# Kernel tuning notes

Measured on AMD Instinct MI355X. Metric: run time of the kernel, lower is better.

Reference implementation:

```python
import jax, jax.numpy as jnp
import numpy as np

D_MODEL = 1024
D_STATE = 16
EXPAND = 2
D_INNER = EXPAND * D_MODEL
DT_RANK = 64  # ceil(1024/16)
D_CONV = 4


def setup_inputs() -> dict:
    key = jax.random.key(0)
    ks = jax.random.split(key, 8)
    s = 0.02
    x = jax.random.normal(ks[0], (2, 2048, D_MODEL), dtype=jnp.float32)
    W_in = jax.random.normal(ks[1], (D_MODEL, 2 * D_INNER), dtype=jnp.float32) * s
    W_conv = jax.random.normal(ks[2], (D_CONV, D_INNER), dtype=jnp.float32) * s  # depthwise taps
    b_conv = jnp.zeros((D_INNER,), dtype=jnp.float32)
    W_xproj = jax.random.normal(ks[3], (D_INNER, DT_RANK + 2 * D_STATE), dtype=jnp.float32) * s
    W_dt = jax.random.normal(ks[4], (DT_RANK, D_INNER), dtype=jnp.float32) * s
    b_dt = jnp.zeros((D_INNER,), dtype=jnp.float32)
    A_log = jnp.broadcast_to(jnp.log(jnp.arange(1, D_STATE + 1, dtype=jnp.float32)), (D_INNER, D_STATE))
    D = jnp.ones((D_INNER,), dtype=jnp.float32)
    W_out = jax.random.normal(ks[5], (D_INNER, D_MODEL), dtype=jnp.float32) * s
    return {"x": x, "W_in": W_in, "W_conv": W_conv, "b_conv": b_conv,
            "W_xproj": W_xproj, "W_dt": W_dt, "b_dt": b_dt,
            "A_log": A_log, "D": D, "W_out": W_out}


def _silu(v):
    return v * jax.nn.sigmoid(v)


def reference(x, W_in, W_conv, b_conv, W_xproj, W_dt, b_dt, A_log, D, W_out):
    B_, L, _ = x.shape
    xz = x @ W_in                     # [B, L, 2*d_inner]
    x_in, z = jnp.split(xz, 2, axis=-1)
    # causal depthwise conv1d (torch padding=d_conv-1 then slice to seq_len)
    pad = D_CONV - 1
    x_pad = jnp.pad(x_in, ((0, 0), (pad, 0), (0, 0)))
    x_conv = b_conv
    x_conv = sum(x_pad[:, k:k + L, :] * W_conv[k] for k in range(D_CONV)) + b_conv
    x_in = _silu(x_conv)              # [B, L, d_inner]
    dbc = x_in @ W_xproj
    dt = jax.nn.softplus(dbc[..., :DT_RANK] @ W_dt + b_dt)   # [B, L, d_inner]
    Bm = dbc[..., DT_RANK:DT_RANK + D_STATE]                  # [B, L, d_state]
    Cm = dbc[..., DT_RANK + D_STATE:]                          # [B, L, d_state]
    A = -jnp.exp(A_log)                                        # [d_inner, d_state]

    def step(state, inp):
        x_t, dt_t, B_t, C_t = inp   # [B,d_inner], [B,d_inner], [B,d_state], [B,d_state]
        dA = jnp.exp(jnp.clip(dt_t[:, :, None] * A[None], -10.0, 10.0))
        dB = dt_t[:, :, None] * B_t[:, None, :]
        state = jnp.clip(state * dA + x_t[:, :, None] * dB, -10.0, 10.0)
        y_t = jnp.einsum('bdn,bn->bd', state, C_t) + D * x_t
        return state, y_t

    tm = lambda a: jnp.swapaxes(a, 0, 1)  # time-major
    state0 = jnp.zeros((B_, D_INNER, D_STATE), dtype=x.dtype)
    _, ys = jax.lax.scan(step, state0, (tm(x_in), tm(dt), tm(Bm), tm(Cm)))
    y = jnp.swapaxes(ys, 0, 1)            # [B, L, d_inner]
    y = y * _silu(z)
    return y @ W_out                       # [B, L, d_model]
```

## Files before the change

### kernel.cpp

```cpp
#include <hip/hip_runtime.h>
#include <math.h>

#define D_MODEL 1024
#define D_INNER 2048
#define D_STATE 16
#define DT_RANK 64
#define LSEQ 2048
#define NBATCH 2
#define M_TOT (NBATCH * LSEQ)
#define DBC_STRIDE 128
#define CH 64
#define NCH (LSEQ / CH)
#define KSPL 8
#define OKSPL 2

typedef unsigned short ushort_t;
typedef unsigned int uint_t;
typedef __attribute__((ext_vector_type(8))) short bf16x8;
typedef __attribute__((ext_vector_type(4))) float f32x4;

__device__ __forceinline__ ushort_t f2bf_rne(float f) {
    uint_t u = __float_as_uint(f);
    u += 0x7fffu + ((u >> 16) & 1u);
    return (ushort_t)(u >> 16);
}
__device__ __forceinline__ float bf2f(ushort_t h) {
    return __uint_as_float(((uint_t)h) << 16);
}

template <int MODE, int TERMS>
__global__ __launch_bounds__(256) void gemm_bf16s(
    const ushort_t* __restrict__ Ah, const ushort_t* __restrict__ Al,
    const ushort_t* __restrict__ BTh, const ushort_t* __restrict__ BTl,
    float* __restrict__ C, float* __restrict__ AUX, int M, int N, int K)
{
    __shared__ __align__(16) ushort_t smem[4 * 128 * 32];
    ushort_t* sAh = smem;
    ushort_t* sAl = smem + 4096;
    ushort_t* sBh = smem + 8192;
    ushort_t* sBl = smem + 12288;
    const int tid = threadIdx.x;
    const int lane = tid & 63;
    const int m0 = blockIdx.y * 128;
    int ks = 0, nblk = blockIdx.x;
    if (MODE == 3) { ks = blockIdx.x; nblk = 0; }
    if (MODE == 4) { ks = blockIdx.x >> 3; nblk = blockIdx.x & 7; }
    const int n0 = nblk * 128;
    const int wave = tid >> 6;
    const int mw = (wave & 1) * 64, nw = (wave >> 1) * 64;
    const int fm = lane & 15, fk = lane >> 4;
    const int swz = fk ^ ((fm >> 1) & 3);

    f32x4 acc[4][4] = {};

    const int r_st0 = tid >> 2, cp0 = tid & 3;
    const int r_st1 = (256 + tid) >> 2, cp1 = tid & 3;
    const int cl0 = cp0 ^ ((r_st0 >> 1) & 3);
    const int cl1 = cp1 ^ ((r_st1 >> 1) & 3);
    const int ldsb0 = (tid & ~63) * 16;
    const int ldsb1 = (256 + (tid & ~63)) * 16;

    const int kbeg = (MODE == 3) ? ks * (K / KSPL)
                   : (MODE == 4) ? ks * (K / OKSPL) : 0;
    const int kend = (MODE == 3) ? kbeg + K / KSPL
                   : (MODE == 4) ? kbeg + K / OKSPL : K;

    for (int k0 = kbeg; k0 < kend; k0 += 32) {
        __syncthreads();
        {
            size_t ga0 = (size_t)(m0 + r_st0) * K + k0 + cl0 * 8;
            size_t ga1 = (size_t)(m0 + r_st1) * K + k0 + cl1 * 8;
            size_t gb0 = (size_t)(n0 + r_st0) * K + k0 + cl0 * 8;
            size_t gb1 = (size_t)(n0 + r_st1) * K + k0 + cl1 * 8;
            __builtin_amdgcn_global_load_lds(
                (const __attribute__((address_space(1))) void*)(Ah + ga0),
                (__attribute__((address_space(3))) void*)((char*)sAh + ldsb0), 16, 0, 0);
            __builtin_amdgcn_global_load_lds(
                (const __attribute__((address_space(1))) void*)(Ah + ga1),
                (__attribute__((address_space(3))) void*)((char*)sAh + ldsb1), 16, 0, 0);
            if (TERMS >= 3) {
                __builtin_amdgcn_global_load_lds(
                    (const __attribute__((address_space(1))) void*)(Al + ga0),
                    (__attribute__((address_space(3))) void*)((char*)sAl + ldsb0), 16, 0, 0);
                __builtin_amdgcn_global_load_lds(
                    (const __attribute__((address_space(1))) void*)(Al + ga1),
                    (__attribute__((address_space(3))) void*)((char*)sAl + ldsb1), 16, 0, 0);
            }
            __builtin_amdgcn_global_load_lds(
                (const __attribute__((address_space(1))) void*)(BTh + gb0),
                (__attribute__((address_space(3))) void*)((char*)sBh + ldsb0), 16, 0, 0);
            __builtin_amdgcn_global_load_lds(
                (const __attribute__((address_space(1))) void*)(BTh + gb1),
                (__attribute__((address_space(3))) void*)((char*)sBh + ldsb1), 16, 0, 0);
            if (TERMS >= 2) {
                __builtin_amdgcn_global_load_lds(
                    (const __attribute__((address_space(1))) void*)(BTl + gb0),
                    (__attribute__((address_space(3))) void*)((char*)sBl + ldsb0), 16, 0, 0);
                __builtin_amdgcn_global_load_lds(
                    (const __attribute__((address_space(1))) void*)(BTl + gb1),
                    (__attribute__((address_space(3))) void*)((char*)sBl + ldsb1), 16, 0, 0);
            }
        }
        __syncthreads();

        bf16x8 fAh[4], fAl[4], fBh[4], fBl[4];
        #pragma unroll
        for (int t = 0; t < 4; ++t) {
            int ra = (mw + t * 16 + fm) * 32 + swz * 8;
            int rb = (nw + t * 16 + fm) * 32 + swz * 8;
            fAh[t] = *reinterpret_cast<const bf16x8*>(&sAh[ra]);
            if (TERMS >= 3) fAl[t] = *reinterpret_cast<const bf16x8*>(&sAl[ra]);
            fBh[t] = *reinterpret_cast<const bf16x8*>(&sBh[rb]);
            if (TERMS >= 2) fBl[t] = *reinterpret_cast<const bf16x8*>(&sBl[rb]);
        }
        #pragma unroll
        for (int i = 0; i < 4; ++i)
            #pragma unroll
            for (int j = 0; j < 4; ++j) {
                acc[i][j] = __builtin_amdgcn_mfma_f32_16x16x32_bf16(fAh[i], fBh[j], acc[i][j], 0, 0, 0);
                if (TERMS >= 3)
                    acc[i][j] = __builtin_amdgcn_mfma_f32_16x16x32_bf16(fAl[i], fBh[j], acc[i][j], 0, 0, 0);
                if (TERMS >= 2)
                    acc[i][j] = __builtin_amdgcn_mfma_f32_16x16x32_bf16(fAh[i], fBl[j], acc[i][j], 0, 0, 0);
            }
    }

    float* Cq = (MODE == 3 || MODE == 4) ? C + (size_t)ks * M * N : C;
    #pragma unroll
    for (int i = 0; i < 4; ++i) {
        int row0 = m0 + mw + i * 16 + fk * 4;
        #pragma unroll
        for (int j = 0; j < 4; ++j) {
            int col = n0 + nw + j * 16 + fm;
            if (MODE == 2) {
                if (col < D_INNER) {
                    #pragma unroll
                    for (int r = 0; r < 4; ++r)
                        C[(size_t)(row0 + r) * D_INNER + col] = acc[i][j][r];
                } else {
                    float4 v = make_float4(acc[i][j][0], acc[i][j][1],
                                           acc[i][j][2], acc[i][j][3]);
                    *reinterpret_cast<float4*>(
                        &AUX[(size_t)(col - D_INNER) * M + row0]) = v;
                }
            } else if (MODE == 5) {
                const float* bias = (const float*)AUX;
                float bc_ = bias[col];
                f32x4 v;
                #pragma unroll
                for (int r = 0; r < 4; ++r) {
                    float t = acc[i][j][r] + bc_;
                    v[r] = fmaxf(t, 0.f) + log1pf(__expf(-fabsf(t)));
                }
                *reinterpret_cast<f32x4*>(&C[(size_t)col * M + row0]) = v;
            } else {
                #pragma unroll
                for (int r = 0; r < 4; ++r)
                    Cq[(size_t)(row0 + r) * N + col] = acc[i][j][r];
            }
        }
    }
}

__global__ __launch_bounds__(256) void xproj_red_k(
    const float* __restrict__ dbcp, float* __restrict__ dbc,
    float* __restrict__ BCT, ushort_t* __restrict__ dbch)
{
    int g = blockIdx.x * 256 + threadIdx.x;
    int m = g >> 7, c = g & 127;
    float s = 0.f;
    #pragma unroll
    for (int ks = 0; ks < KSPL; ++ks)
        s += dbcp[(size_t)ks * M_TOT * DBC_STRIDE + g];
    dbc[g] = s;
    if (c < 64)
        dbch[(size_t)m * 64 + c] = f2bf_rne(s);
    else if (c < 96)
        BCT[(size_t)(c - 64) * M_TOT + m] = s;
}

__global__ __launch_bounds__(256) void outred_k(
    const float* __restrict__ p, float* __restrict__ out)
{
    int i4 = (blockIdx.x * 256 + threadIdx.x) * 4;
    f32x4 a = *reinterpret_cast<const f32x4*>(p + i4);
    f32x4 b = *reinterpret_cast<const f32x4*>(p + (size_t)M_TOT * D_MODEL + i4);
    *reinterpret_cast<f32x4*>(out + i4) = a + b;
}

__global__ __launch_bounds__(256) void cast_h_k(
    const float* __restrict__ X, ushort_t* __restrict__ Xh)
{
    int i4 = (blockIdx.x * 256 + threadIdx.x) * 4;
    float4 v = *reinterpret_cast<const float4*>(X + i4);
    ushort2 a = make_ushort2(f2bf_rne(v.x), f2bf_rne(v.y));
    ushort2 b = make_ushort2(f2bf_rne(v.z), f2bf_rne(v.w));
    *reinterpret_cast<ushort2*>(Xh + i4)     = a;
    *reinterpret_cast<ushort2*>(Xh + i4 + 2) = b;
}

__global__ __launch_bounds__(256) void transpose_cast_k(
    const float* __restrict__ W, ushort_t* __restrict__ Th, ushort_t* __restrict__ Tl,
    int K, int N)
{
    __shared__ float tile[32][33];
    int n0 = blockIdx.x * 32, k0 = blockIdx.y * 32;
    int tx = threadIdx.x & 31, ty = threadIdx.x >> 5;
    #pragma unroll
    for (int i = 0; i < 32; i += 8)
        tile[ty + i][tx] = W[(size_t)(k0 + ty + i) * N + n0 + tx];
    __syncthreads();
    #pragma unroll
    for (int i = 0; i < 32; i += 8) {
        float v = tile[tx][ty + i];
        ushort_t h = f2bf_rne(v);
        ushort_t l = f2bf_rne(v - bf2f(h));
        size_t o = (size_t)(n0 + ty + i) * K + k0 + tx;
        Th[o] = h; Tl[o] = l;
    }
}

__global__ __launch_bounds__(256) void transpose_cast_pad_k(
    const float* __restrict__ W, ushort_t* __restrict__ Th, int K, int N)
{
    __shared__ float tile[32][33];
    int n0 = blockIdx.x * 32, k0 = blockIdx.y * 32;
    int tx = threadIdx.x & 31, ty = threadIdx.x >> 5;
    #pragma unroll
    for (int i = 0; i < 32; i += 8)
        tile[ty + i][tx] = (n0 + tx < N) ? W[(size_t)(k0 + ty + i) * N + n0 + tx] : 0.f;
    __syncthreads();
    #pragma unroll
    for (int i = 0; i < 32; i += 8) {
        float v = tile[tx][ty + i];
        size_t o = (size_t)(n0 + ty + i) * K + k0 + tx;
        Th[o] = f2bf_rne(v);
    }
}

__global__ __launch_bounds__(256) void conv_silu_k(
    const float* __restrict__ xbuf, const float* __restrict__ Wc,
    const float* __restrict__ bc, ushort_t* __restrict__ xinh,
    float* __restrict__ xT)
{
    __shared__ float tile[67][64];
    const int c0 = blockIdx.x * 64;
    const int m0 = blockIdx.y * 64;
    const int bstart = m0 & ~(LSEQ - 1);
    const int tid = threadIdx.x;

    for (int e = tid; e < 67 * 64; e += 256) {
        int r = e >> 6, c = e & 63;
        int g = m0 - 3 + r;
        tile[r][c] = (g >= bstart) ? xbuf[(size_t)g * D_INNER + c0 + c] : 0.f;
    }
    __syncthreads();

    const int c_l = tid & 63, mg = tid >> 6;
    const int c = c0 + c_l;
    const float w0 = Wc[c], w1 = Wc[D_INNER + c];
    const float w2 = Wc[2 * D_INNER + c], w3 = Wc[3 * D_INNER + c];
    const float bb = bc[c];
    float xtbuf[16];
    #pragma unroll
    for (int mi = 0; mi < 16; ++mi) {
        int r = mg * 16 + mi;
        float acc = bb + tile[r][c_l] * w0 + tile[r + 1][c_l] * w1
                       + tile[r + 2][c_l] * w2 + tile[r + 3][c_l] * w3;
        float sv = acc / (1.f + __expf(-acc));
        xinh[(size_t)(m0 + r) * D_INNER + c] = f2bf_rne(sv);
        xtbuf[mi] = sv;
    }
    float* xtp = xT + (size_t)c * M_TOT + m0 + mg * 16;
    #pragma unroll
    for (int q = 0; q < 4; ++q)
        *reinterpret_cast<float4*>(xtp + 4 * q) =
            make_float4(xtbuf[4 * q], xtbuf[4 * q + 1], xtbuf[4 * q + 2], xtbuf[4 * q + 3]);
}

__global__ __launch_bounds__(256) void scan_sum_k(
    const float* __restrict__ dtT, const float* __restrict__ xT,
    const float* __restrict__ BCT, const float* __restrict__ A_log,
    float* __restrict__ asumb, float* __restrict__ sendb)
{
    __shared__ float sdt[16][68], sx[16][68], sBs[16][68];
    const int tid = threadIdx.x;
    const int c0 = blockIdx.x << 4;
    const int ck = blockIdx.y;
    const int b  = blockIdx.z;
    const size_t boff = (size_t)b * LSEQ + ck * CH;

    {
        int r = tid >> 4, q = (tid & 15) << 2;
        *reinterpret_cast<float4*>(&sdt[r][q]) =
            *reinterpret_cast<const float4*>(dtT + (size_t)(c0 + r) * M_TOT + boff + q);
        *reinterpret_cast<float4*>(&sx[r][q]) =
            *reinterpret_cast<const float4*>(xT + (size_t)(c0 + r) * M_TOT + boff + q);
        *reinterpret_cast<float4*>(&sBs[r][q]) =
            *reinterpret_cast<const float4*>(BCT + (size_t)r * M_TOT + boff + q);
    }
    __syncthreads();

    const int n = tid & 15, ch = tid >> 4;
    const int d = c0 + ch;
    const float Adn = -__expf(A_log[d * D_STATE + n]);
    float s = 0.f, asum = 0.f;
    #pragma unroll 4
    for (int tq = 0; tq < CH / 4; ++tq) {
        f32x4 dv = *reinterpret_cast<const f32x4*>(&sdt[ch][tq * 4]);
        f32x4 xv = *reinterpret_cast<const f32x4*>(&sx[ch][tq * 4]);
        f32x4 Bv = *reinterpret_cast<const f32x4*>(&sBs[n][tq * 4]);
        #pragma unroll
        for (int j = 0; j < 4; ++j) {
            float a = fminf(fmaxf(dv[j] * Adn, -10.f), 10.f);
            asum += a;
            float e = __expf(a);
            float t = s * e + dv[j] * xv[j] * Bv[j];
            s = fminf(fmaxf(t, -10.f), 10.f);
        }
    }
    size_t idx = (((size_t)(b * NCH + ck) * D_INNER) + d) * D_STATE + n;
    asumb[idx] = asum;
    sendb[idx] = s;
}

__global__ __launch_bounds__(256) void scan_fix_k(
    const float* __restrict__ asumb, const float* __restrict__ sendb,
    float* __restrict__ sinb)
{
    int g = blockIdx.x * 256 + threadIdx.x;
    int n = g & 15, d = (g >> 4) & (D_INNER - 1), b = g >> 15;
    float s = 0.f;
    for (int ck = 0; ck < NCH; ++ck) {
        size_t idx = (((size_t)(b * NCH + ck) * D_INNER) + d) * D_STATE + n;
        sinb[idx] = s;
        float t = s * __expf(asumb[idx]) + sendb[idx];
        s = fminf(fmaxf(t, -10.f), 10.f);
    }
}

__global__ __launch_bounds__(256) void scan_apply_k(
    const float* __restrict__ dtT, const float* __restrict__ xT,
    const float* __restrict__ BCT, const float* __restrict__ zT,
    const float* __restrict__ sinb,
    const float* __restrict__ A_log, const float* __restrict__ Dv,
    ushort_t* __restrict__ Yh)
{
    __shared__ float sdt[16][68], sx[16][68], sBs[16][68], sCs[16][68], sz[16][68];
    __shared__ float ps[4][16 * 68];
    const int tid = threadIdx.x;
    const int c0 = blockIdx.x << 4;
    const int ck = blockIdx.y;
    const int b  = blockIdx.z;
    const size_t boff = (size_t)b * LSEQ + ck * CH;

    {
        int r = tid >> 4, q = (tid & 15) << 2;
        *reinterpret_cast<float4*>(&sdt[r][q]) =
            *reinterpret_cast<const float4*>(dtT + (size_t)(c0 + r) * M_TOT + boff + q);
        *reinterpret_cast<float4*>(&sx[r][q]) =
            *reinterpret_cast<const float4*>(xT + (size_t)(c0 + r) * M_TOT + boff + q);
        *reinterpret_cast<float4*>(&sBs[r][q]) =
            *reinterpret_cast<const float4*>(BCT + (size_t)r * M_TOT + boff + q);
        *reinterpret_cast<float4*>(&sCs[r][q]) =
            *reinterpret_cast<const float4*>(BCT + (size_t)(16 + r) * M_TOT + boff + q);
        *reinterpret_cast<float4*>(&sz[r][q]) =
            *reinterpret_cast<const float4*>(zT + (size_t)(c0 + r) * M_TOT + boff + q);
    }
    __syncthreads();

    const int w = tid >> 6, lane = tid & 63;
    const int n = lane & 15, cl = lane >> 4;
    const int t_r = lane >> 2, cl_r = lane & 3;
    const int chs = w * 4 + cl;
    const int d = c0 + chs;
    const int cho = w * 4 + cl_r;
    const int d_out = c0 + cho;
    const float Adn = -__expf(A_log[d * D_STATE + n]);
    const float DdEff = (n == 0) ? Dv[d] : 0.f;
    float s = sinb[(((size_t)(b * NCH + ck) * D_INNER) + d) * D_STATE + n];

    #pragma unroll
    for (int tg = 0; tg < CH / 16; ++tg) {
        #pragma unroll
        for (int tq = 0; tq < 4; ++tq) {
            int t4 = tg * 16 + tq * 4;
            f32x4 dv = *reinterpret_cast<const f32x4*>(&sdt[chs][t4]);
            f32x4 xv = *reinterpret_cast<const f32x4*>(&sx[chs][t4]);
            f32x4 Bv = *reinterpret_cast<const f32x4*>(&sBs[n][t4]);
            f32x4 Cv = *reinterpret_cast<const f32x4*>(&sCs[n][t4]);
            #pragma unroll
            for (int j = 0; j < 4; ++j) {
                float a = fminf(fmaxf(dv[j] * Adn, -10.f), 10.f);
                float e = __expf(a);
                float t = s * e + dv[j] * xv[j] * Bv[j];
                s = fminf(fmaxf(t, -10.f), 10.f);
                ps[w][(tq * 4 + j) * 68 + cl * 16 + n] = s * Cv[j] + DdEff * xv[j];
            }
        }
        __builtin_amdgcn_wave_barrier();
        {
            const float* pb = &ps[w][t_r * 68 + cl_r * 16];
            f32x4 r0 = *reinterpret_cast<const f32x4*>(pb + 0);
            f32x4 r1 = *reinterpret_cast<const f32x4*>(pb + 4);
            f32x4 r2 = *reinterpret_cast<const f32x4*>(pb + 8);
            f32x4 r3 = *reinterpret_cast<const f32x4*>(pb + 12);
            f32x4 sv4 = (r0 + r1) + (r2 + r3);
            float sum = (sv4[0] + sv4[1]) + (sv4[2] + sv4[3]);
            float zz = sz[cho][tg * 16 + t_r];
            float szg = zz / (1.f + __expf(-zz));
            float val = sum * szg;
            size_t om = (boff + tg * 16 + t_r) * D_INNER + d_out;
            Yh[om] = f2bf_rne(val);
        }
        __builtin_amdgcn_wave_barrier();
    }
}

extern "C" void kernel_launch(void* const* d_in, const int* in_sizes, int n_in,
                              void* d_out, int out_size, void* d_ws, size_t ws_size,
                              hipStream_t stream)
{
    const float* x       = (const float*)d_in[0];
    const float* W_in    = (const float*)d_in[1];
    const float* W_conv  = (const float*)d_in[2];
    const float* b_conv  = (const float*)d_in[3];
    const float* W_xproj = (const float*)d_in[4];
    const float* W_dt    = (const float*)d_in[5];
    const float* b_dt    = (const float*)d_in[6];
    const float* A_log   = (const float*)d_in[7];
    const float* Dv      = (const float*)d_in[8];
    const float* W_out   = (const float*)d_in[9];
    float* out = (float*)d_out;

    float* xbuf = (float*)d_ws;
    float* zT   = xbuf + (size_t)M_TOT * D_INNER;
    float* dbc  = zT + (size_t)D_INNER * M_TOT;
    float* BCT  = dbc + (size_t)M_TOT * DBC_STRIDE;
    ushort_t* xh     = (ushort_t*)(BCT + (size_t)32 * M_TOT);
    ushort_t* xl     = xh + (size_t)M_TOT * D_MODEL;
    ushort_t* WinTh  = xl + (size_t)M_TOT * D_MODEL;
    ushort_t* WinTl  = WinTh + (size_t)2 * D_INNER * D_MODEL;
    ushort_t* WoutTh = WinTl + (size_t)2 * D_INNER * D_MODEL;
    ushort_t* WoutTl = WoutTh + (size_t)D_MODEL * D_INNER;
    ushort_t* WxTh   = WoutTl + (size_t)D_MODEL * D_INNER;
    ushort_t* WxTl   = WxTh + (size_t)DBC_STRIDE * D_INNER;
    ushort_t* xinh   = WxTl + (size_t)DBC_STRIDE * D_INNER;
    ushort_t* xinl   = xinh + (size_t)M_TOT * D_INNER;
    ushort_t* yh     = xinl + (size_t)M_TOT * D_INNER;
    ushort_t* yl     = yh + (size_t)M_TOT * D_INNER;
    ushort_t* WdtTh  = yl + (size_t)M_TOT * D_INNER;
    ushort_t* dbch   = WdtTh + (size_t)D_INNER * DT_RANK;
    float* xT   = (float*)xh;
    float* dtT  = (float*)xinh;
    float* dbcp = (float*)yh;
    float* pout = (float*)xh;
    const size_t NSUM = (size_t)NBATCH * NCH * D_INNER * D_STATE;
    float* asumb = xbuf;
    float* sendb = xbuf + NSUM;
    float* sinb  = xbuf + 2 * NSUM;

    cast_h_k<<<(M_TOT * D_MODEL) / 1024, 256, 0, stream>>>(x, xh);
    transpose_cast_pad_k<<<dim3((2 * D_INNER) / 32, D_MODEL / 32), 256, 0, stream>>>(
        W_in, WinTh, D_MODEL, 2 * D_INNER);
    transpose_cast_k<<<dim3(D_MODEL / 32, D_INNER / 32), 256, 0, stream>>>(
        W_out, WoutTh, WoutTl, D_INNER, D_MODEL);
    transpose_cast_pad_k<<<dim3(DBC_STRIDE / 32, D_INNER / 32), 256, 0, stream>>>(
        W_xproj, WxTh, D_INNER, DT_RANK + 2 * D_STATE);
    transpose_cast_pad_k<<<dim3(D_INNER / 32, DT_RANK / 32), 256, 0, stream>>>(
        W_dt, WdtTh, DT_RANK, D_INNER);

    gemm_bf16s<2, 1><<<dim3(32, 32), 256, 0, stream>>>(
        xh, nullptr, WinTh, nullptr, xbuf, zT, M_TOT, 2 * D_INNER, D_MODEL);
    conv_silu_k<<<dim3(D_INNER / 64, M_TOT / 64), 256, 0, stream>>>(
        xbuf, W_conv, b_conv, xinh, xT);
    gemm_bf16s<3, 1><<<dim3(KSPL, 32), 256, 0, stream>>>(
        xinh, nullptr, WxTh, nullptr, dbcp, nullptr, M_TOT, DBC_STRIDE, D_INNER);
    xproj_red_k<<<(M_TOT * DBC_STRIDE) / 256, 256, 0, stream>>>(dbcp, dbc, BCT, dbch);
    gemm_bf16s<5, 1><<<dim3(D_INNER / 128, M_TOT / 128), 256, 0, stream>>>(
        dbch, nullptr, WdtTh, nullptr, dtT, (float*)b_dt, M_TOT, D_INNER, DT_RANK);
    scan_sum_k<<<dim3(D_INNER / 16, NCH, NBATCH), 256, 0, stream>>>(
        dtT, xT, BCT, A_log, asumb, sendb);
    scan_fix_k<<<(NBATCH * D_INNER * D_STATE) / 256, 256, 0, stream>>>(
        asumb, sendb, sinb);
    scan_apply_k<<<dim3(D_INNER / 16, NCH, NBATCH), 256, 0, stream>>>(
        dtT, xT, BCT, zT, sinb, A_log, Dv, yh);
    gemm_bf16s<4, 2><<<dim3(OKSPL * 8, 32), 256, 0, stream>>>(
        yh, nullptr, WoutTh, WoutTl, pout, nullptr, M_TOT, D_MODEL, D_INNER);
    outred_k<<<(M_TOT * D_MODEL) / 1024, 256, 0, stream>>>(pout, out);
}
```

Before: 380.9 us.

## Replace in-projection GEMM with 256x256-tile pipelined kernel using direct global-to-LDS loads

The input projection GEMM (4096x4096x1024, bf16 single term) moves from the generic 128x128 kernel to a dedicated 512-thread kernel with 256x256 tiles. It streams operands into LDS with global_load_lds in a double-buffered, multi-stage pipeline, using swizzled LDS layout, explicit vmcnt/lgkmcnt waits and setprio around MFMA bursts. The aim is more operand reuse per tile, with global loads overlapping the matrix math. In exchange it uses 128KB of LDS and only 256 blocks, and the hand-tuned wait counts are fragile.

```diff
diff --git a/kernel.cpp b/kernel.cpp
--- a/kernel.cpp
+++ b/kernel.cpp
@@ -26,6 +26,177 @@
 }
 __device__ __forceinline__ float bf2f(ushort_t h) {
     return __uint_as_float(((uint_t)h) << 16);
+}
+
+#define KIN 1024
+#define KTI (KIN / 64)
+
+#define BAR()   __builtin_amdgcn_s_barrier()
+#define LGKM0() asm volatile("s_waitcnt lgkmcnt(0)" ::: "memory")
+
+#define LDFRAG_B(SRC)                                                          \
+    _Pragma("unroll")                                                          \
+    for (int nf = 0; nf < 4; ++nf)                                             \
+        fB[nf] = *reinterpret_cast<const bf16x8*>(                             \
+            &(SRC)[(bRow + nf * 16 + fm) * 32 + swz * 8]);
+
+#define LDFRAG_A(SRC, MOFF)                                                    \
+    _Pragma("unroll")                                                          \
+    for (int mf = 0; mf < 4; ++mf)                                             \
+        fA[mf] = *reinterpret_cast<const bf16x8*>(                             \
+            &(SRC)[(aRow + (MOFF + mf) * 16 + fm) * 32 + swz * 8]);
+
+#define MFMA_QUAD(MOFF)                                                        \
+    __builtin_amdgcn_s_setprio(1);                                             \
+    _Pragma("unroll")                                                          \
+    for (int mf = 0; mf < 4; ++mf)                                             \
+        _Pragma("unroll")                                                      \
+        for (int nf = 0; nf < 4; ++nf)                                         \
+            acc[MOFF + mf][nf] = __builtin_amdgcn_mfma_f32_16x16x32_bf16(      \
+                fA[mf], fB[nf], acc[MOFF + mf][nf], 0, 0, 0);                  \
+    __builtin_amdgcn_s_setprio(0);
+
+__global__ __launch_bounds__(512, 2) void gemm256_inproj(
+    const ushort_t* __restrict__ Ah, const ushort_t* __restrict__ BTh,
+    float* __restrict__ C, float* __restrict__ AUX)
+{
+    __shared__ __align__(1024) ushort_t smem[65536];
+    const int tid  = threadIdx.x;
+    const int lane = tid & 63;
+    const int w    = tid >> 6;
+    const int wm   = w >> 2;
+    const int wn   = w & 3;
+    const int fm   = lane & 15, fk = lane >> 4;
+    const int swz  = fk ^ ((fm >> 1) & 3);
+    const int aRow = wm * 128;
+    const int bRow = wn * 64;
+    const int m0   = blockIdx.y * 256;
+    const int n0   = blockIdx.x * 256;
+    const int rbase = w * 16 + (lane >> 2);
+    const int ssw   = ((lane & 3) ^ ((lane >> 3) & 3)) * 8;
+
+    f32x4 acc[8][4] = {};
+
+    auto stage = [&](const ushort_t* __restrict__ g, int grow0, int kcol,
+                     int regUS) {
+        #pragma unroll
+        for (int q = 0; q < 2; ++q) {
+            const ushort_t* src =
+                g + (size_t)(grow0 + q * 128 + rbase) * KIN + kcol + ssw;
+            __builtin_amdgcn_global_load_lds(
+                (const __attribute__((address_space(1))) void*)src,
+                (__attribute__((address_space(3))) void*)(smem + regUS +
+                                                          q * 4096 + w * 512),
+                16, 0, 0);
+        }
+    };
+
+    stage(Ah,  m0, 0,  0);
+    stage(BTh, n0, 0,  32768);
+    stage(Ah,  m0, 32, 8192);
+    stage(BTh, n0, 32, 32768 + 8192);
+    stage(Ah,  m0, 64, 16384);
+    stage(BTh, n0, 64, 32768 + 16384);
+    asm volatile("s_waitcnt vmcnt(8)" ::: "memory");
+    BAR();
+
+    bf16x8 fA[4], fB[4];
+
+    for (int t = 0; t < KTI - 1; ++t) {
+        const int bf = t & 1, bn = bf ^ 1;
+        const ushort_t* A0 = smem + (bf * 2 + 0) * 8192;
+        const ushort_t* A1 = smem + (bf * 2 + 1) * 8192;
+        const ushort_t* B0 = smem + 32768 + (bf * 2 + 0) * 8192;
+        const ushort_t* B1 = smem + 32768 + (bf * 2 + 1) * 8192;
+        const int kc1 = (t + 1) * 64, kc2 = (t + 2) * 64;
+        const bool st2 = (t + 2 < KTI);
+
+        LDFRAG_B(B0);
+        LDFRAG_A(A0, 0);
+        stage(Ah, m0, kc1 + 32, (bn * 2 + 1) * 8192);
+        BAR(); LGKM0();
+        MFMA_QUAD(0);
+        BAR();
+
+        LDFRAG_A(A0, 4);
+        stage(BTh, n0, kc1 + 32, 32768 + (bn * 2 + 1) * 8192);
+        BAR(); LGKM0();
+        MFMA_QUAD(4);
+        asm volatile("s_waitcnt vmcnt(8)" ::: "memory");
+        BAR();
+        __builtin_amdgcn_sched_barrier(0);
+
+        LDFRAG_B(B1);
+        LDFRAG_A(A1, 0);
+        if (st2) stage(Ah, m0, kc2, (bf * 2 + 0) * 8192);
+        BAR(); LGKM0();
+        MFMA_QUAD(0);
+        BAR();
+
+        LDFRAG_A(A1, 4);
+        if (st2) stage(BTh, n0, kc2, 32768 + (bf * 2 + 0) * 8192);
+        BAR(); LGKM0();
+        MFMA_QUAD(4);
+        if (t == KTI - 2) { asm volatile("s_waitcnt vmcnt(4)" ::: "memory"); }
+        else              { asm volatile("s_waitcnt vmcnt(6)" ::: "memory"); }
+        BAR();
+        __builtin_amdgcn_sched_barrier(0);
+    }
+
+    {
+        const int bf = (KTI - 1) & 1;
+        const ushort_t* A0 = smem + (bf * 2 + 0) * 8192;
+        const ushort_t* A1 = smem + (bf * 2 + 1) * 8192;
+        const ushort_t* B0 = smem + 32768 + (bf * 2 + 0) * 8192;
+        const ushort_t* B1 = smem + 32768 + (bf * 2 + 1) * 8192;
+
+        LDFRAG_B(B0);
+        LDFRAG_A(A0, 0);
+        BAR(); LGKM0();
+        MFMA_QUAD(0);
+        BAR();
+
+        LDFRAG_A(A0, 4);
+        BAR(); LGKM0();
+        MFMA_QUAD(4);
+        asm volatile("s_waitcnt vmcnt(0)" ::: "memory");
+        BAR();
+
+        LDFRAG_B(B1);
+        LDFRAG_A(A1, 0);
+        BAR(); LGKM0();
+        MFMA_QUAD(0);
+        BAR();
+
+        LDFRAG_A(A1, 4);
+        BAR(); LGKM0();
+        MFMA_QUAD(4);
+    }
+
+    if (n0 < D_INNER) {
+        #pragma unroll
+        for (int mf = 0; mf < 8; ++mf) {
+            int row0 = m0 + aRow + mf * 16 + fk * 4;
+            #pragma unroll
+            for (int nf = 0; nf < 4; ++nf) {
+                int col = n0 + bRow + nf * 16 + fm;
+                #pragma unroll
+                for (int r = 0; r < 4; ++r)
+                    C[(size_t)(row0 + r) * D_INNER + col] = acc[mf][nf][r];
+            }
+        }
+    } else {
+        #pragma unroll
+        for (int mf = 0; mf < 8; ++mf) {
+            int row0 = m0 + aRow + mf * 16 + fk * 4;
+            #pragma unroll
+            for (int nf = 0; nf < 4; ++nf) {
+                int col = n0 + bRow + nf * 16 + fm;
+                *reinterpret_cast<f32x4*>(
+                    &AUX[(size_t)(col - D_INNER) * M_TOT + row0]) = acc[mf][nf];
+            }
+        }
+    }
 }
 
 template <int MODE, int TERMS>
@@ -132,18 +303,7 @@
         #pragma unroll
         for (int j = 0; j < 4; ++j) {
             int col = n0 + nw + j * 16 + fm;
-            if (MODE == 2) {
-                if (col < D_INNER) {
-                    #pragma unroll
-                    for (int r = 0; r < 4; ++r)
-                        C[(size_t)(row0 + r) * D_INNER + col] = acc[i][j][r];
-                } else {
-                    float4 v = make_float4(acc[i][j][0], acc[i][j][1],
-                                           acc[i][j][2], acc[i][j][3]);
-                    *reinterpret_cast<float4*>(
-                        &AUX[(size_t)(col - D_INNER) * M + row0]) = v;
-                }
-            } else if (MODE == 5) {
+            if (MODE == 5) {
                 const float* bias = (const float*)AUX;
                 float bc_ = bias[col];
                 f32x4 v;
@@ -470,8 +630,7 @@
     transpose_cast_pad_k<<<dim3(D_INNER / 32, DT_RANK / 32), 256, 0, stream>>>(
         W_dt, WdtTh, DT_RANK, D_INNER);
 
-    gemm_bf16s<2, 1><<<dim3(32, 32), 256, 0, stream>>>(
-        xh, nullptr, WinTh, nullptr, xbuf, zT, M_TOT, 2 * D_INNER, D_MODEL);
+    gemm256_inproj<<<dim3(16, 16), 512, 0, stream>>>(xh, WinTh, xbuf, zT);
     conv_silu_k<<<dim3(D_INNER / 64, M_TOT / 64), 256, 0, stream>>>(
         xbuf, W_conv, b_conv, xinh, xT);
     gemm_bf16s<3, 1><<<dim3(KSPL, 32), 256, 0, stream>>>(
```

New measurement: 359.2 us. -5.7%, faster.
